# Performance work log

Measured on AMD Instinct MI355X. Metric: run time of the kernel, lower is better.

Reference implementation:

```python
import jax, jax.numpy as jnp
import numpy as np

EMBED, HEADS, FF, WIN = 512, 8, 2048, 64
SIGMA, PSTRENGTH, PERIOD, THRESH = 2.0, 1.0, 100.0, 0.0


def layer_norm(x, g, b, eps=1e-5):
    mu = jnp.mean(x, axis=-1, keepdims=True)
    var = jnp.var(x, axis=-1, keepdims=True)
    return (x - mu) * jax.lax.rsqrt(var + eps) * g + b


def setup_inputs() -> dict:
    key = jax.random.key(0)
    ks = jax.random.split(key, 16)
    s = 1.0 / np.sqrt(EMBED)
    sf = 1.0 / np.sqrt(FF)
    inp = {
        "src": jax.random.normal(ks[0], (8, 2048, EMBED), dtype=jnp.float32),
        "Wq": jax.random.normal(ks[1], (EMBED, EMBED), dtype=jnp.float32) * s,
        "bq": jnp.zeros((EMBED,), jnp.float32),
        "Wk": jax.random.normal(ks[2], (EMBED, EMBED), dtype=jnp.float32) * s,
        "bk": jnp.zeros((EMBED,), jnp.float32),
        "Wv": jax.random.normal(ks[3], (EMBED, EMBED), dtype=jnp.float32) * s,
        "bv": jnp.zeros((EMBED,), jnp.float32),
        "Wo": jax.random.normal(ks[4], (EMBED, EMBED), dtype=jnp.float32) * s,
        "bo": jnp.zeros((EMBED,), jnp.float32),
        "Wg": jax.random.normal(ks[5], (EMBED, 1), dtype=jnp.float32) * s,
        "bg": jnp.zeros((1,), jnp.float32),
        "W1": jax.random.normal(ks[6], (EMBED, FF), dtype=jnp.float32) * s,
        "b1": jnp.zeros((FF,), jnp.float32),
        "W2": jax.random.normal(ks[7], (FF, EMBED), dtype=jnp.float32) * sf,
        "b2": jnp.zeros((EMBED,), jnp.float32),
        "ln1_g": jnp.ones((EMBED,), jnp.float32),
        "ln1_b": jnp.zeros((EMBED,), jnp.float32),
        "ln2_g": jnp.ones((EMBED,), jnp.float32),
        "ln2_b": jnp.zeros((EMBED,), jnp.float32),
    }
    return inp


def gated_sparse_attn(x, Wq, bq, Wk, bk, Wv, bv, Wo, bo, Wg, bg):
    B, S, D = x.shape
    H, dh = HEADS, D // HEADS
    q = (x @ Wq + bq).reshape(B, S, H, dh).transpose(0, 2, 1, 3)  # [B,H,S,dh]
    k = (x @ Wk + bk).reshape(B, S, H, dh).transpose(0, 2, 1, 3)
    v = (x @ Wv + bv).reshape(B, S, H, dh).transpose(0, 2, 1, 3)
    scores = jnp.einsum('bhqd,bhkd->bhqk', q, k) / jnp.sqrt(jnp.float32(dh))
    idx = jnp.arange(S, dtype=jnp.float32)
    dist = idx[:, None] - idx[None, :]  # [S,S]
    gauss_bias = jnp.exp(-(dist * dist) / (2.0 * SIGMA * SIGMA))
    per_bias = PSTRENGTH * jnp.cos(2.0 * jnp.pi * dist / PERIOD)
    scores = scores + gauss_bias + per_bias  # positional biases baked into scores
    local = jnp.abs(dist) <= WIN  # local-window sparsity mask
    scores = jnp.where(local, scores, jnp.float32(-1e9))
    attn = jax.nn.softmax(scores, axis=-1)
    out = jnp.einsum('bhqk,bhkd->bhqd', attn, v)
    out = out.transpose(0, 2, 1, 3).reshape(B, S, D) @ Wo + bo
    gate = jax.nn.sigmoid(x @ Wg + bg)  # [B,S,1] learned gating
    gate = jnp.where(gate > THRESH, gate, jnp.float32(0.0))
    return gate * out


def reference(src, Wq, bq, Wk, bk, Wv, bv, Wo, bo, Wg, bg, W1, b1, W2, b2, ln1_g, ln1_b, ln2_g, ln2_b):
    # dropout is identity in eval mode
    attn_out = gated_sparse_attn(src, Wq, bq, Wk, bk, Wv, bv, Wo, bo, Wg, bg)
    x = layer_norm(src + attn_out, ln1_g, ln1_b)
    ff = jax.nn.relu(x @ W1 + b1) @ W2 + b2
    return layer_norm(x + ff, ln2_g, ln2_b)
```

## Files before the change

kernel.cpp:

```cpp
#include <hip/hip_runtime.h>
#include <hip/hip_bf16.h>
#include <math.h>

#define S_LEN   2048
#define D_MOD   512
#define N_HEADS 8
#define D_HEAD  64
#define FF_DIM  2048
#define M_ROWS  16384
#define BHSD    8388608

typedef __attribute__((ext_vector_type(8))) __bf16 bf16x8;
typedef __attribute__((ext_vector_type(4))) float  f32x4;
typedef unsigned short u16;

__device__ __forceinline__ u16 f2bf(float f) {
  unsigned u = __float_as_uint(f);
  u += 0x7fffu + ((u >> 16) & 1u);
  return (u16)(u >> 16);
}
__device__ __forceinline__ float bf2f(u16 h) { return __uint_as_float(((unsigned)h) << 16); }

__device__ __forceinline__ f32x4 mfma16(bf16x8 a, bf16x8 b, f32x4 c) {
  return __builtin_amdgcn_mfma_f32_16x16x32_bf16(a, b, c, 0, 0, 0);
}

__device__ __forceinline__ void async16(void* lds, const void* g) {
  __builtin_amdgcn_global_load_lds(
      (const __attribute__((address_space(1))) unsigned int*)g,
      (__attribute__((address_space(3))) unsigned int*)lds, 16, 0, 0);
}

#define BAR()    asm volatile("s_barrier" ::: "memory")
#define WAITV(n) asm volatile("s_waitcnt vmcnt(" #n ")" ::: "memory")
#define WAITL()  asm volatile("s_waitcnt lgkmcnt(0)" ::: "memory")

__device__ __forceinline__ int swz384(int row, int bir) {
  return row * 384 + ((bir & ~127) | ((bir ^ ((row & 7) << 4)) & 127));
}

__global__ __launch_bounds__(256) void cvt_gate(const float* __restrict__ src,
                                                const float* __restrict__ Wg,
                                                const float* __restrict__ bg,
                                                u16* __restrict__ xb,
                                                float* __restrict__ gate) {
  const int wid = threadIdx.x >> 6, lane = threadIdx.x & 63;
  const size_t row = (size_t)blockIdx.x * 4 + wid;
  const float4* s = reinterpret_cast<const float4*>(src + row * D_MOD);
  const float4* w = reinterpret_cast<const float4*>(Wg);
  float4 a0 = s[lane * 2], a1 = s[lane * 2 + 1];
  float4 w0 = w[lane * 2], w1 = w[lane * 2 + 1];
  float acc = a0.x * w0.x + a0.y * w0.y + a0.z * w0.z + a0.w * w0.w +
              a1.x * w1.x + a1.y * w1.y + a1.z * w1.z + a1.w * w1.w;
#pragma unroll
  for (int m = 1; m < 64; m <<= 1) acc += __shfl_xor(acc, m);
  ushort4 h0, h1;
  h0.x = f2bf(a0.x); h0.y = f2bf(a0.y); h0.z = f2bf(a0.z); h0.w = f2bf(a0.w);
  h1.x = f2bf(a1.x); h1.y = f2bf(a1.y); h1.z = f2bf(a1.z); h1.w = f2bf(a1.w);
  ushort4* ob = reinterpret_cast<ushort4*>(xb + row * D_MOD);
  ob[lane * 2] = h0; ob[lane * 2 + 1] = h1;
  if (lane == 0) {
    float g = 1.f / (1.f + __expf(-(acc + bg[0])));
    gate[row] = g > 0.f ? g : 0.f;
  }
}

__global__ void transpose_cvt(const float* __restrict__ in, u16* __restrict__ out,
                              int K, int N) {
  __shared__ float t[32][33];
  const int n0 = blockIdx.x * 32, k0 = blockIdx.y * 32;
  const int tx = threadIdx.x, ty = threadIdx.y;
#pragma unroll
  for (int i = 0; i < 4; ++i)
    t[ty + 8 * i][tx] = in[(size_t)(k0 + ty + 8 * i) * N + n0 + tx];
  __syncthreads();
#pragma unroll
  for (int i = 0; i < 4; ++i)
    out[(size_t)(n0 + ty + 8 * i) * K + k0 + tx] = f2bf(t[tx][ty + 8 * i]);
}

__global__ __launch_bounds__(256) void ln1red_k(const u16* __restrict__ xb,
                                                const float* __restrict__ gate,
                                                const u16* __restrict__ p0,
                                                const u16* __restrict__ p1,
                                                const float* __restrict__ bo,
                                                const float* __restrict__ gam,
                                                const float* __restrict__ bet,
                                                u16* __restrict__ outb) {
  const int wid = threadIdx.x >> 6, lane = threadIdx.x & 63;
  const size_t row = (size_t)blockIdx.x * 4 + wid;
  const size_t base = row * D_MOD;
  const float g = gate[row];
  const ushort4* sp = reinterpret_cast<const ushort4*>(xb + base);
  const ushort4* a  = reinterpret_cast<const ushort4*>(p0 + base);
  const ushort4* c  = reinterpret_cast<const ushort4*>(p1 + base);
  const float4*  bb = reinterpret_cast<const float4*>(bo);
  ushort4 s0 = sp[lane * 2], s1 = sp[lane * 2 + 1];
  ushort4 a0 = a[lane * 2], a1 = a[lane * 2 + 1];
  ushort4 c0 = c[lane * 2], c1 = c[lane * 2 + 1];
  float4 d0 = bb[lane * 2], d1 = bb[lane * 2 + 1];
  float4 v0, v1;
  v0.x = bf2f(s0.x) + g * (bf2f(a0.x) + bf2f(c0.x) + d0.x);
  v0.y = bf2f(s0.y) + g * (bf2f(a0.y) + bf2f(c0.y) + d0.y);
  v0.z = bf2f(s0.z) + g * (bf2f(a0.z) + bf2f(c0.z) + d0.z);
  v0.w = bf2f(s0.w) + g * (bf2f(a0.w) + bf2f(c0.w) + d0.w);
  v1.x = bf2f(s1.x) + g * (bf2f(a1.x) + bf2f(c1.x) + d1.x);
  v1.y = bf2f(s1.y) + g * (bf2f(a1.y) + bf2f(c1.y) + d1.y);
  v1.z = bf2f(s1.z) + g * (bf2f(a1.z) + bf2f(c1.z) + d1.z);
  v1.w = bf2f(s1.w) + g * (bf2f(a1.w) + bf2f(c1.w) + d1.w);
  float s  = v0.x + v0.y + v0.z + v0.w + v1.x + v1.y + v1.z + v1.w;
  float s2 = v0.x * v0.x + v0.y * v0.y + v0.z * v0.z + v0.w * v0.w +
             v1.x * v1.x + v1.y * v1.y + v1.z * v1.z + v1.w * v1.w;
#pragma unroll
  for (int m = 1; m < 64; m <<= 1) { s += __shfl_xor(s, m); s2 += __shfl_xor(s2, m); }
  const float mu = s * (1.0f / 512.0f);
  const float var = s2 * (1.0f / 512.0f) - mu * mu;
  const float rs = 1.0f / sqrtf(var + 1e-5f);
  const float4* gp = reinterpret_cast<const float4*>(gam);
  const float4* bp = reinterpret_cast<const float4*>(bet);
  float4 g0 = gp[lane * 2], g1 = gp[lane * 2 + 1];
  float4 e0 = bp[lane * 2], e1 = bp[lane * 2 + 1];
  ushort4 h0, h1;
  h0.x = f2bf((v0.x - mu) * rs * g0.x + e0.x);  h0.y = f2bf((v0.y - mu) * rs * g0.y + e0.y);
  h0.z = f2bf((v0.z - mu) * rs * g0.z + e0.z);  h0.w = f2bf((v0.w - mu) * rs * g0.w + e0.w);
  h1.x = f2bf((v1.x - mu) * rs * g1.x + e1.x);  h1.y = f2bf((v1.y - mu) * rs * g1.y + e1.y);
  h1.z = f2bf((v1.z - mu) * rs * g1.z + e1.z);  h1.w = f2bf((v1.w - mu) * rs * g1.w + e1.w);
  ushort4* ob = reinterpret_cast<ushort4*>(outb + base);
  ob[lane * 2] = h0; ob[lane * 2 + 1] = h1;
}

__global__ __launch_bounds__(256) void ln2red_k(const u16* __restrict__ xb,
                                                const u16* __restrict__ p0,
                                                const u16* __restrict__ p1,
                                                const float* __restrict__ b2,
                                                const float* __restrict__ gam,
                                                const float* __restrict__ bet,
                                                float* __restrict__ out) {
  const int wid = threadIdx.x >> 6, lane = threadIdx.x & 63;
  const size_t row = (size_t)blockIdx.x * 4 + wid;
  const size_t base = row * D_MOD;
  const ushort4* xp = reinterpret_cast<const ushort4*>(xb + base);
  const ushort4* q0 = reinterpret_cast<const ushort4*>(p0 + base);
  const ushort4* q1 = reinterpret_cast<const ushort4*>(p1 + base);
  const float4* bb = reinterpret_cast<const float4*>(b2);
  ushort4 h0 = xp[lane * 2], h1 = xp[lane * 2 + 1];
  ushort4 a0 = q0[lane * 2], a1 = q0[lane * 2 + 1];
  ushort4 c0 = q1[lane * 2], c1 = q1[lane * 2 + 1];
  float4 d0 = bb[lane * 2], d1 = bb[lane * 2 + 1];
  float4 v0, v1;
  v0.x = bf2f(h0.x) + bf2f(a0.x) + bf2f(c0.x) + d0.x;
  v0.y = bf2f(h0.y) + bf2f(a0.y) + bf2f(c0.y) + d0.y;
  v0.z = bf2f(h0.z) + bf2f(a0.z) + bf2f(c0.z) + d0.z;
  v0.w = bf2f(h0.w) + bf2f(a0.w) + bf2f(c0.w) + d0.w;
  v1.x = bf2f(h1.x) + bf2f(a1.x) + bf2f(c1.x) + d1.x;
  v1.y = bf2f(h1.y) + bf2f(a1.y) + bf2f(c1.y) + d1.y;
  v1.z = bf2f(h1.z) + bf2f(a1.z) + bf2f(c1.z) + d1.z;
  v1.w = bf2f(h1.w) + bf2f(a1.w) + bf2f(c1.w) + d1.w;
  float s  = v0.x + v0.y + v0.z + v0.w + v1.x + v1.y + v1.z + v1.w;
  float s2 = v0.x * v0.x + v0.y * v0.y + v0.z * v0.z + v0.w * v0.w +
             v1.x * v1.x + v1.y * v1.y + v1.z * v1.z + v1.w * v1.w;
#pragma unroll
  for (int m = 1; m < 64; m <<= 1) { s += __shfl_xor(s, m); s2 += __shfl_xor(s2, m); }
  const float mu = s * (1.0f / 512.0f);
  const float var = s2 * (1.0f / 512.0f) - mu * mu;
  const float rs = 1.0f / sqrtf(var + 1e-5f);
  const float4* gp = reinterpret_cast<const float4*>(gam);
  const float4* bp = reinterpret_cast<const float4*>(bet);
  float4 g0 = gp[lane * 2], g1 = gp[lane * 2 + 1];
  float4 e0 = bp[lane * 2], e1 = bp[lane * 2 + 1];
  float4 o0, o1;
  o0.x = (v0.x - mu) * rs * g0.x + e0.x;  o0.y = (v0.y - mu) * rs * g0.y + e0.y;
  o0.z = (v0.z - mu) * rs * g0.z + e0.z;  o0.w = (v0.w - mu) * rs * g0.w + e0.w;
  o1.x = (v1.x - mu) * rs * g1.x + e1.x;  o1.y = (v1.y - mu) * rs * g1.y + e1.y;
  o1.z = (v1.z - mu) * rs * g1.z + e1.z;  o1.w = (v1.w - mu) * rs * g1.w + e1.w;
  float4* q = reinterpret_cast<float4*>(out + base);
  q[lane * 2] = o0; q[lane * 2 + 1] = o1;
}

struct EpiArgs {
  const float* b0; const float* b1; const float* b2;
  float* outf; u16* outb; u16* outb2;
};

template<int EPI, int LD, int NT, int KSLICE, int GX, int GY>
__device__ __forceinline__ void gemm256_body(const u16* __restrict__ A,
                                             const u16* __restrict__ Bt, EpiArgs e) {
  extern __shared__ char smem[];
  char* Asb = smem;
  char* Bsb = smem + 65536;
  const int tid = threadIdx.x;
  const int wid = tid >> 6, lane = tid & 63;
  const int sub = lane >> 4, lc = lane & 15;
  const int wr = wid >> 2, wcn = wid & 3;

  const int nwg = (int)(gridDim.x * gridDim.y * gridDim.z);
  const int orig = ((int)blockIdx.z * (int)gridDim.y + (int)blockIdx.y) * (int)gridDim.x + (int)blockIdx.x;
  const int cpx = nwg >> 3;
  const int wg = (orig & 7) * cpx + (orig >> 3);
  const int bx = wg % GX;
  const int by = (wg / GX) % GY;
  const int bz = wg / (GX * GY);
  const int m0 = by * 256, n0 = bx * 256;
  const int kb = KSLICE * bz;

  const u16* Ab = A + (size_t)m0 * LD;
  const u16* Bb = Bt + (size_t)n0 * LD;

  f32x4 acc[8][4];
#pragma unroll
  for (int i = 0; i < 8; ++i)
#pragma unroll
    for (int j = 0; j < 4; ++j) acc[i][j] = (f32x4){0.f, 0.f, 0.f, 0.f};

  const int lr0 = tid >> 3;
  const int sl  = tid & 7;

#define STAGE(BASE, SRC, BUF, KT)                                              \
  {                                                                            \
    const int kk_ = kb + (KT) * 64;                                            \
    _Pragma("unroll")                                                          \
    for (int r_ = 0; r_ < 4; ++r_) {                                           \
      const int lr_ = r_ * 64 + lr0;                                           \
      async16((BASE) + (BUF) * 32768 + r_ * 8192 + wid * 1024,                 \
              (SRC) + (size_t)lr_ * LD + kk_ + ((sl ^ (lr_ & 7)) << 3));       \
    }                                                                          \
  }
#define LDFRAG(BASE, ROW, KS) \
  (*reinterpret_cast<const bf16x8*>((BASE) + (ROW) * 128 + ((((KS) * 64) + sub * 16) ^ (((ROW) & 7) << 4))))

  STAGE(Bsb, Bb, 0, 0);
  STAGE(Asb, Ab, 0, 0);
  STAGE(Bsb, Bb, 1, 1);
  STAGE(Asb, Ab, 1, 1);
  WAITV(8);
  BAR();

  for (int t = 0; t < NT; ++t) {
    const int buf = t & 1;
    char* Abl = Asb + buf * 32768;
    char* Bbl = Bsb + buf * 32768;
    bf16x8 af[4][2], bfr[2][2][2];
#pragma unroll
    for (int f = 0; f < 4; ++f) {
      const int row = wr * 128 + f * 16 + lc;
#pragma unroll
      for (int ks = 0; ks < 2; ++ks) af[f][ks] = LDFRAG(Abl, row, ks);
    }
#pragma unroll
    for (int f = 0; f < 2; ++f) {
      const int row = wcn * 64 + f * 16 + lc;
#pragma unroll
      for (int ks = 0; ks < 2; ++ks) bfr[0][f][ks] = LDFRAG(Bbl, row, ks);
    }
    __builtin_amdgcn_s_setprio(1);
#pragma unroll
    for (int f = 0; f < 4; ++f)
#pragma unroll
      for (int c = 0; c < 2; ++c)
#pragma unroll
        for (int ks = 0; ks < 2; ++ks)
          acc[f][c] = mfma16(af[f][ks], bfr[0][c][ks], acc[f][c]);
    __builtin_amdgcn_s_setprio(0);
    BAR();
#pragma unroll
    for (int f = 0; f < 2; ++f) {
      const int row = wcn * 64 + 32 + f * 16 + lc;
#pragma unroll
      for (int ks = 0; ks < 2; ++ks) bfr[1][f][ks] = LDFRAG(Bbl, row, ks);
    }
    __builtin_amdgcn_s_setprio(1);
#pragma unroll
    for (int f = 0; f < 4; ++f)
#pragma unroll
      for (int c = 0; c < 2; ++c)
#pragma unroll
        for (int ks = 0; ks < 2; ++ks)
          acc[f][2 + c] = mfma16(af[f][ks], bfr[1][c][ks], acc[f][2 + c]);
    __builtin_amdgcn_s_setprio(0);
    WAITL();
    BAR();
    if (t + 2 < NT) STAGE(Bsb, Bb, buf, t + 2);
#pragma unroll
    for (int f = 0; f < 4; ++f) {
      const int row = wr * 128 + 64 + f * 16 + lc;
#pragma unroll
      for (int ks = 0; ks < 2; ++ks) af[f][ks] = LDFRAG(Abl, row, ks);
    }
    __builtin_amdgcn_s_setprio(1);
#pragma unroll
    for (int f = 0; f < 4; ++f)
#pragma unroll
      for (int c = 0; c < 2; ++c)
#pragma unroll
        for (int ks = 0; ks < 2; ++ks)
          acc[4 + f][2 + c] = mfma16(af[f][ks], bfr[1][c][ks], acc[4 + f][2 + c]);
    __builtin_amdgcn_s_setprio(0);
    WAITL();
    BAR();
    if (t + 2 < NT) STAGE(Asb, Ab, buf, t + 2);
    __builtin_amdgcn_s_setprio(1);
#pragma unroll
    for (int f = 0; f < 4; ++f)
#pragma unroll
      for (int c = 0; c < 2; ++c)
#pragma unroll
        for (int ks = 0; ks < 2; ++ks)
          acc[4 + f][c] = mfma16(af[f][ks], bfr[0][c][ks], acc[4 + f][c]);
    __builtin_amdgcn_s_setprio(0);
    if (t + 1 < NT) {
      if (t + 2 < NT) { WAITV(8); } else { WAITV(0); }
      BAR();
    }
  }
#undef STAGE
#undef LDFRAG

  if constexpr (EPI == 2 || EPI == 4) {
#pragma unroll
    for (int fr = 0; fr < 8; ++fr) {
      const int row0 = m0 + wr * 128 + fr * 16 + sub * 4;
#pragma unroll
      for (int fc = 0; fc < 4; ++fc) {
        const int col = n0 + wcn * 64 + fc * 16 + lc;
        f32x4 v = acc[fr][fc];
#pragma unroll
        for (int i = 0; i < 4; ++i) {
          const int row = row0 + i;
          const float val = v[i];
          if constexpr (EPI == 2) {
            float o = val + e.b0[col];
            e.outb[(size_t)row * FF_DIM + col] = f2bf(o > 0.f ? o : 0.f);
          } else {
            u16* dst = (bz == 0) ? e.outb : e.outb2;
            dst[(size_t)row * D_MOD + col] = f2bf(val);
          }
        }
      }
    }
  } else {
    const int which = n0 >> 9;
    const int bbi = m0 >> 11, ss0 = m0 & 2047;
    if (which == 2) {
      __syncthreads();
      u16* Cs = reinterpret_cast<u16*>(smem);
      const int nnb = n0 & 511;
#pragma unroll
      for (int fr = 0; fr < 8; ++fr) {
        const int lrow = wr * 128 + fr * 16 + sub * 4;
#pragma unroll
        for (int fc = 0; fc < 4; ++fc) {
          const int lcol = wcn * 64 + fc * 16 + lc;
          const float bias = e.b2[nnb + lcol];
          f32x4 v = acc[fr][fc];
#pragma unroll
          for (int i = 0; i < 4; ++i) {
            const int row = lrow + i;
            const int sbyte = (row * 2) ^ ((lcol & 7) << 4);
            *reinterpret_cast<u16*>((char*)Cs + lcol * 512 + sbyte) = f2bf(v[i] + bias);
          }
        }
      }
      __syncthreads();
#pragma unroll
      for (int p = 0; p < 16; ++p) {
        const int off = p * 8192 + tid * 16;
        const int nn = off >> 9, cb = off & 511;
        const int cbs = cb ^ ((nn & 7) << 4);
        uint4 v = *reinterpret_cast<const uint4*>((const char*)Cs + nn * 512 + cbs);
        const int nng = nnb + nn;
        const int hh = nng >> 6, dd = nng & 63;
        *reinterpret_cast<uint4*>(
            (char*)(e.outb2 + (((size_t)bbi * N_HEADS + hh) * D_HEAD + dd) * S_LEN + ss0) + cb) = v;
      }
    } else {
#pragma unroll
      for (int fr = 0; fr < 8; ++fr) {
        const int row0 = m0 + wr * 128 + fr * 16 + sub * 4;
        const int ss = row0 & 2047;
#pragma unroll
        for (int fc = 0; fc < 4; ++fc) {
          const int col = n0 + wcn * 64 + fc * 16 + lc;
          const int nn = col & 511;
          const int hh = nn >> 6, dd = nn & 63;
          const float* bp = (which == 0) ? e.b0 : e.b1;
          const float bias = bp[nn];
          f32x4 v = acc[fr][fc];
#pragma unroll
          for (int i = 0; i < 4; ++i)
            e.outb[(size_t)which * BHSD +
                   (((size_t)bbi * N_HEADS + hh) * S_LEN + ss + i) * D_HEAD + dd]
                = f2bf(v[i] + bias);
        }
      }
    }
  }
}

__global__ __launch_bounds__(512, 2) void k_qkv(const u16* __restrict__ A, const u16* __restrict__ B, EpiArgs e) {
  gemm256_body<0, 512, 8, 0, 6, 64>(A, B, e);
}
__global__ __launch_bounds__(512, 2) void k_ff1(const u16* __restrict__ A, const u16* __restrict__ B, EpiArgs e) {
  gemm256_body<2, 512, 8, 0, 8, 64>(A, B, e);
}
__global__ __launch_bounds__(512, 2) void k_ff2(const u16* __restrict__ A, const u16* __restrict__ B, EpiArgs e) {
  gemm256_body<4, 2048, 16, 1024, 2, 64>(A, B, e);
}
__global__ __launch_bounds__(512, 2) void k_proj(const u16* __restrict__ A, const u16* __restrict__ B, EpiArgs e) {
  gemm256_body<4, 512, 4, 256, 2, 64>(A, B, e);
}

__global__ __launch_bounds__(256)
void attn_k(const u16* __restrict__ Q, const u16* __restrict__ Kt,
            const u16* __restrict__ VTg, u16* __restrict__ Oflat) {
  __shared__ __align__(16) u16 VT[64 * 192];
  __shared__ __align__(16) u16 P [64 * 192];
  __shared__ float tab[256];
  const int tid = threadIdx.x;
  const int wid = tid >> 6, lane = tid & 63;
  const int sub = lane >> 4, lc = lane & 15;
  const int qb = blockIdx.x, bh = blockIdx.y;
  const int bb = bh >> 3, hh = bh & 7;
  const int q0 = qb * 64, kstart = q0 - 64;
  const u16* Qb = Q  + (size_t)bh * S_LEN * D_HEAD;
  const u16* Kb = Kt + (size_t)bh * S_LEN * D_HEAD;
  const u16* Vtb = VTg + (size_t)bh * D_HEAD * S_LEN;

#pragma unroll
  for (int it = 0; it < 6; ++it) {
    const int c = (wid * 6 + it) * 64 + lane;
    const int row = c / 24;
    const int bir = (c % 24) * 16;
    const int swz = (bir & ~127) | ((bir ^ ((row & 7) << 4)) & 127);
    int sb = kstart + (swz >> 1);
    sb = sb < 0 ? 0 : (sb > S_LEN - 8 ? S_LEN - 8 : sb);
    async16((char*)VT + (wid * 6 + it) * 1024, Vtb + (size_t)row * S_LEN + sb);
  }

  if (tid < 255) {
    const int di = tid - 127;
    const float fd = (float)di;
    tab[tid] = (di >= -64 && di <= 64)
        ? __expf(-fd * fd * 0.125f) + __cosf(0.06283185307179586f * fd)
        : -1e9f;
  }

  bf16x8 qf[2];
#pragma unroll
  for (int ks = 0; ks < 2; ++ks)
    qf[ks] = *reinterpret_cast<const bf16x8*>(Qb + (size_t)(q0 + wid * 16 + lc) * D_HEAD + ks * 32 + sub * 8);

  f32x4 sc[12];
#pragma unroll
  for (int t = 0; t < 12; ++t) sc[t] = (f32x4){0.f, 0.f, 0.f, 0.f};
#pragma unroll
  for (int ks = 0; ks < 2; ++ks)
#pragma unroll
    for (int t = 0; t < 12; ++t) {
      int kg = kstart + t * 16 + lc;
      int kc = kg < 0 ? 0 : (kg > S_LEN - 1 ? S_LEN - 1 : kg);
      bf16x8 kf = *reinterpret_cast<const bf16x8*>(Kb + (size_t)kc * D_HEAD + ks * 32 + sub * 8);
      sc[t] = mfma16(qf[ks], kf, sc[t]);
    }
  __syncthreads();

  float rmax[4] = {-3e38f, -3e38f, -3e38f, -3e38f};
#pragma unroll
  for (int t = 0; t < 12; ++t) {
    const int kk = t * 16 + lc;
    const int kg = kstart + kk;
    const bool valid = (kg >= 0) && (kg < S_LEN);
#pragma unroll
    for (int r = 0; r < 4; ++r) {
      const int qrow = wid * 16 + sub * 4 + r;
      const float bias = valid ? tab[qrow - kk + 191] : -1e9f;
      const float sv = sc[t][r] * 0.125f + bias;
      sc[t][r] = sv;
      rmax[r] = fmaxf(rmax[r], sv);
    }
  }
#pragma unroll
  for (int m = 1; m < 16; m <<= 1)
#pragma unroll
    for (int r = 0; r < 4; ++r) rmax[r] = fmaxf(rmax[r], __shfl_xor(rmax[r], m));
  float rsum[4] = {0.f, 0.f, 0.f, 0.f};
#pragma unroll
  for (int t = 0; t < 12; ++t)
#pragma unroll
    for (int r = 0; r < 4; ++r) {
      const float p = __expf(sc[t][r] - rmax[r]);
      sc[t][r] = p; rsum[r] += p;
    }
#pragma unroll
  for (int m = 1; m < 16; m <<= 1)
#pragma unroll
    for (int r = 0; r < 4; ++r) rsum[r] += __shfl_xor(rsum[r], m);
  float rinv[4];
#pragma unroll
  for (int r = 0; r < 4; ++r) rinv[r] = 1.0f / rsum[r];
#pragma unroll
  for (int t = 0; t < 12; ++t)
#pragma unroll
    for (int r = 0; r < 4; ++r) {
      const int qrow = wid * 16 + sub * 4 + r;
      *reinterpret_cast<u16*>(reinterpret_cast<char*>(P) + swz384(qrow, (t * 16 + lc) * 2))
          = f2bf(sc[t][r] * rinv[r]);
    }
  __syncthreads();

  f32x4 oacc[4];
#pragma unroll
  for (int t = 0; t < 4; ++t) oacc[t] = (f32x4){0.f, 0.f, 0.f, 0.f};
  const int arow = wid * 16 + lc;
#pragma unroll
  for (int ks = 0; ks < 6; ++ks) {
    const int bir = ks * 64 + sub * 16;
    bf16x8 pa = *reinterpret_cast<const bf16x8*>(reinterpret_cast<char*>(P) + swz384(arow, bir));
#pragma unroll
    for (int t = 0; t < 4; ++t) {
      bf16x8 vb = *reinterpret_cast<const bf16x8*>(reinterpret_cast<char*>(VT) + swz384(t * 16 + lc, bir));
      oacc[t] = mfma16(pa, vb, oacc[t]);
    }
  }

  const size_t obase = ((size_t)bb * S_LEN + q0) * D_MOD + hh * D_HEAD;
#pragma unroll
  for (int t = 0; t < 4; ++t)
#pragma unroll
    for (int r = 0; r < 4; ++r) {
      const int qrow = wid * 16 + sub * 4 + r;
      Oflat[obase + (size_t)qrow * D_MOD + t * 16 + lc] = f2bf(oacc[t][r]);
    }
}

extern "C" void kernel_launch(void* const* d_in, const int* in_sizes, int n_in,
                              void* d_out, int out_size, void* d_ws, size_t ws_size,
                              hipStream_t stream) {
  (void)in_sizes; (void)n_in; (void)out_size; (void)ws_size;
  const float* src  = (const float*)d_in[0];
  const float* Wq   = (const float*)d_in[1];
  const float* bq   = (const float*)d_in[2];
  const float* Wk   = (const float*)d_in[3];
  const float* bk   = (const float*)d_in[4];
  const float* Wv   = (const float*)d_in[5];
  const float* bv   = (const float*)d_in[6];
  const float* Wo   = (const float*)d_in[7];
  const float* bo   = (const float*)d_in[8];
  const float* Wg   = (const float*)d_in[9];
  const float* bg   = (const float*)d_in[10];
  const float* W1   = (const float*)d_in[11];
  const float* b1   = (const float*)d_in[12];
  const float* W2   = (const float*)d_in[13];
  const float* b2   = (const float*)d_in[14];
  const float* ln1g = (const float*)d_in[15];
  const float* ln1b = (const float*)d_in[16];
  const float* ln2g = (const float*)d_in[17];
  const float* ln2b = (const float*)d_in[18];
  float* out = (float*)d_out;

  char* ws = (char*)d_ws;
  u16*   WqkvT  = (u16*)  (ws + 0);
  u16*   WoT    = (u16*)  (ws + 1572864);
  u16*   W1T    = (u16*)  (ws + 2097152);
  u16*   W2T    = (u16*)  (ws + 4194304);
  float* gatef  = (float*)(ws + 6291456);
  u16*   Xbf    = (u16*)  (ws + 6356992);
  u16*   QKVbf  = (u16*)  (ws + 23134208);
  u16*   attnfl = (u16*)  (ws + 73465856);
  u16*   pr0    = (u16*)  (ws + 90243072);
  u16*   pr1    = (u16*)  (ws + 107020288);
  u16*   xbf2   = (u16*)  (ws + 123797504);
  u16*   VTg    = (u16*)  (ws + 140574720);
  u16*   hbuf   = Xbf;
  u16*   pf0    = pr0;
  u16*   pf1    = pr1;

  (void)hipFuncSetAttribute((const void*)k_qkv,  hipFuncAttributeMaxDynamicSharedMemorySize, 131072);
  (void)hipFuncSetAttribute((const void*)k_ff1,  hipFuncAttributeMaxDynamicSharedMemorySize, 131072);
  (void)hipFuncSetAttribute((const void*)k_ff2,  hipFuncAttributeMaxDynamicSharedMemorySize, 131072);
  (void)hipFuncSetAttribute((const void*)k_proj, hipFuncAttributeMaxDynamicSharedMemorySize, 131072);

  dim3 tb(32, 8);
  cvt_gate<<<4096, 256, 0, stream>>>(src, Wg, bg, Xbf, gatef);
  transpose_cvt<<<dim3(16, 16), tb, 0, stream>>>(Wq, WqkvT,             512, 512);
  transpose_cvt<<<dim3(16, 16), tb, 0, stream>>>(Wk, WqkvT + 512 * 512, 512, 512);
  transpose_cvt<<<dim3(16, 16), tb, 0, stream>>>(Wv, WqkvT + 2 * 512 * 512, 512, 512);
  transpose_cvt<<<dim3(16, 16), tb, 0, stream>>>(Wo, WoT, 512, 512);
  transpose_cvt<<<dim3(64, 16), tb, 0, stream>>>(W1, W1T, 512, 2048);
  transpose_cvt<<<dim3(16, 64), tb, 0, stream>>>(W2, W2T, 2048, 512);

  EpiArgs e1{bq, bk, bv, nullptr, QKVbf, VTg};
  k_qkv<<<dim3(6, 64, 1), 512, 131072, stream>>>(Xbf, WqkvT, e1);

  attn_k<<<dim3(32, 64), 256, 0, stream>>>(QKVbf, QKVbf + BHSD, VTg, attnfl);

  EpiArgs e2{nullptr, nullptr, nullptr, nullptr, pr0, pr1};
  k_proj<<<dim3(2, 64, 2), 512, 131072, stream>>>(attnfl, WoT, e2);

  ln1red_k<<<4096, 256, 0, stream>>>(Xbf, gatef, pr0, pr1, bo, ln1g, ln1b, xbf2);

  EpiArgs e3{b1, nullptr, nullptr, nullptr, hbuf, nullptr};
  k_ff1<<<dim3(8, 64, 1), 512, 131072, stream>>>(xbf2, W1T, e3);

  EpiArgs e4{nullptr, nullptr, nullptr, nullptr, pf0, pf1};
  k_ff2<<<dim3(2, 64, 2), 512, 131072, stream>>>(hbuf, W2T, e4);

  ln2red_k<<<4096, 256, 0, stream>>>(xbf2, pf0, pf1, b2, ln2g, ln2b, out);
}
```

Baseline: 215.5 us.

## Add single-buffered GEMM variant with 64KB LDS for higher occupancy in proj/FF

Adds a DBUF template flag to the 256x256 GEMM body. The new single-buffered path stages one K-tile, waits, computes, then loads the next tile. k_proj, k_ff1 and k_ff2 now use it with 64KB dynamic LDS and launch_bounds(512,4), trading intra-block load/compute overlap for more resident workgroups per CU. The risk is exposed global-load latency and register pressure under the tighter occupancy bound, since 128 accumulator floats per thread may spill.

```diff
diff --git a/kernel.cpp b/kernel.cpp
--- a/kernel.cpp
+++ b/kernel.cpp
@@ -182,12 +182,12 @@
   float* outf; u16* outb; u16* outb2;
 };
 
-template<int EPI, int LD, int NT, int KSLICE, int GX, int GY>
+template<int EPI, int LD, int NT, int KSLICE, int GX, int GY, int DBUF>
 __device__ __forceinline__ void gemm256_body(const u16* __restrict__ A,
                                              const u16* __restrict__ Bt, EpiArgs e) {
   extern __shared__ char smem[];
   char* Asb = smem;
-  char* Bsb = smem + 65536;
+  char* Bsb = smem + (DBUF ? 65536 : 32768);
   const int tid = threadIdx.x;
   const int wid = tid >> 6, lane = tid & 63;
   const int sub = lane >> 4, lc = lane & 15;
@@ -228,88 +228,137 @@
 #define LDFRAG(BASE, ROW, KS) \
   (*reinterpret_cast<const bf16x8*>((BASE) + (ROW) * 128 + ((((KS) * 64) + sub * 16) ^ (((ROW) & 7) << 4))))
 
-  STAGE(Bsb, Bb, 0, 0);
-  STAGE(Asb, Ab, 0, 0);
-  STAGE(Bsb, Bb, 1, 1);
-  STAGE(Asb, Ab, 1, 1);
-  WAITV(8);
-  BAR();
-
-  for (int t = 0; t < NT; ++t) {
-    const int buf = t & 1;
-    char* Abl = Asb + buf * 32768;
-    char* Bbl = Bsb + buf * 32768;
-    bf16x8 af[4][2], bfr[2][2][2];
-#pragma unroll
-    for (int f = 0; f < 4; ++f) {
-      const int row = wr * 128 + f * 16 + lc;
-#pragma unroll
-      for (int ks = 0; ks < 2; ++ks) af[f][ks] = LDFRAG(Abl, row, ks);
-    }
-#pragma unroll
-    for (int f = 0; f < 2; ++f) {
-      const int row = wcn * 64 + f * 16 + lc;
-#pragma unroll
-      for (int ks = 0; ks < 2; ++ks) bfr[0][f][ks] = LDFRAG(Bbl, row, ks);
-    }
-    __builtin_amdgcn_s_setprio(1);
-#pragma unroll
-    for (int f = 0; f < 4; ++f)
-#pragma unroll
-      for (int c = 0; c < 2; ++c)
-#pragma unroll
-        for (int ks = 0; ks < 2; ++ks)
-          acc[f][c] = mfma16(af[f][ks], bfr[0][c][ks], acc[f][c]);
-    __builtin_amdgcn_s_setprio(0);
+  if constexpr (DBUF) {
+    STAGE(Bsb, Bb, 0, 0);
+    STAGE(Asb, Ab, 0, 0);
+    STAGE(Bsb, Bb, 1, 1);
+    STAGE(Asb, Ab, 1, 1);
+    WAITV(8);
     BAR();
-#pragma unroll
-    for (int f = 0; f < 2; ++f) {
-      const int row = wcn * 64 + 32 + f * 16 + lc;
-#pragma unroll
-      for (int ks = 0; ks < 2; ++ks) bfr[1][f][ks] = LDFRAG(Bbl, row, ks);
-    }
-    __builtin_amdgcn_s_setprio(1);
-#pragma unroll
-    for (int f = 0; f < 4; ++f)
-#pragma unroll
-      for (int c = 0; c < 2; ++c)
-#pragma unroll
-        for (int ks = 0; ks < 2; ++ks)
-          acc[f][2 + c] = mfma16(af[f][ks], bfr[1][c][ks], acc[f][2 + c]);
-    __builtin_amdgcn_s_setprio(0);
-    WAITL();
-    BAR();
-    if (t + 2 < NT) STAGE(Bsb, Bb, buf, t + 2);
-#pragma unroll
-    for (int f = 0; f < 4; ++f) {
-      const int row = wr * 128 + 64 + f * 16 + lc;
-#pragma unroll
-      for (int ks = 0; ks < 2; ++ks) af[f][ks] = LDFRAG(Abl, row, ks);
-    }
-    __builtin_amdgcn_s_setprio(1);
-#pragma unroll
-    for (int f = 0; f < 4; ++f)
-#pragma unroll
-      for (int c = 0; c < 2; ++c)
-#pragma unroll
-        for (int ks = 0; ks < 2; ++ks)
-          acc[4 + f][2 + c] = mfma16(af[f][ks], bfr[1][c][ks], acc[4 + f][2 + c]);
-    __builtin_amdgcn_s_setprio(0);
-    WAITL();
-    BAR();
-    if (t + 2 < NT) STAGE(Asb, Ab, buf, t + 2);
-    __builtin_amdgcn_s_setprio(1);
-#pragma unroll
-    for (int f = 0; f < 4; ++f)
-#pragma unroll
-      for (int c = 0; c < 2; ++c)
-#pragma unroll
-        for (int ks = 0; ks < 2; ++ks)
-          acc[4 + f][c] = mfma16(af[f][ks], bfr[0][c][ks], acc[4 + f][c]);
-    __builtin_amdgcn_s_setprio(0);
-    if (t + 1 < NT) {
-      if (t + 2 < NT) { WAITV(8); } else { WAITV(0); }
+
+    for (int t = 0; t < NT; ++t) {
+      const int buf = t & 1;
+      char* Abl = Asb + buf * 32768;
+      char* Bbl = Bsb + buf * 32768;
+      bf16x8 af[4][2], bfr[2][2][2];
+#pragma unroll
+      for (int f = 0; f < 4; ++f) {
+        const int row = wr * 128 + f * 16 + lc;
+#pragma unroll
+        for (int ks = 0; ks < 2; ++ks) af[f][ks] = LDFRAG(Abl, row, ks);
+      }
+#pragma unroll
+      for (int f = 0; f < 2; ++f) {
+        const int row = wcn * 64 + f * 16 + lc;
+#pragma unroll
+        for (int ks = 0; ks < 2; ++ks) bfr[0][f][ks] = LDFRAG(Bbl, row, ks);
+      }
+      __builtin_amdgcn_s_setprio(1);
+#pragma unroll
+      for (int f = 0; f < 4; ++f)
+#pragma unroll
+        for (int c = 0; c < 2; ++c)
+#pragma unroll
+          for (int ks = 0; ks < 2; ++ks)
+            acc[f][c] = mfma16(af[f][ks], bfr[0][c][ks], acc[f][c]);
+      __builtin_amdgcn_s_setprio(0);
       BAR();
+#pragma unroll
+      for (int f = 0; f < 2; ++f) {
+        const int row = wcn * 64 + 32 + f * 16 + lc;
+#pragma unroll
+        for (int ks = 0; ks < 2; ++ks) bfr[1][f][ks] = LDFRAG(Bbl, row, ks);
+      }
+      __builtin_amdgcn_s_setprio(1);
+#pragma unroll
+      for (int f = 0; f < 4; ++f)
+#pragma unroll
+        for (int c = 0; c < 2; ++c)
+#pragma unroll
+          for (int ks = 0; ks < 2; ++ks)
+            acc[f][2 + c] = mfma16(af[f][ks], bfr[1][c][ks], acc[f][2 + c]);
+      __builtin_amdgcn_s_setprio(0);
+      WAITL();
+      BAR();
+      if (t + 2 < NT) STAGE(Bsb, Bb, buf, t + 2);
+#pragma unroll
+      for (int f = 0; f < 4; ++f) {
+        const int row = wr * 128 + 64 + f * 16 + lc;
+#pragma unroll
+        for (int ks = 0; ks < 2; ++ks) af[f][ks] = LDFRAG(Abl, row, ks);
+      }
+      __builtin_amdgcn_s_setprio(1);
+#pragma unroll
+      for (int f = 0; f < 4; ++f)
+#pragma unroll
+        for (int c = 0; c < 2; ++c)
+#pragma unroll
+          for (int ks = 0; ks < 2; ++ks)
+            acc[4 + f][2 + c] = mfma16(af[f][ks], bfr[1][c][ks], acc[4 + f][2 + c]);
+      __builtin_amdgcn_s_setprio(0);
+      WAITL();
+      BAR();
+      if (t + 2 < NT) STAGE(Asb, Ab, buf, t + 2);
+      __builtin_amdgcn_s_setprio(1);
+#pragma unroll
+      for (int f = 0; f < 4; ++f)
+#pragma unroll
+        for (int c = 0; c < 2; ++c)
+#pragma unroll
+          for (int ks = 0; ks < 2; ++ks)
+            acc[4 + f][c] = mfma16(af[f][ks], bfr[0][c][ks], acc[4 + f][c]);
+      __builtin_amdgcn_s_setprio(0);
+      if (t + 1 < NT) {
+        if (t + 2 < NT) { WAITV(8); } else { WAITV(0); }
+        BAR();
+      }
+    }
+  } else {
+    STAGE(Bsb, Bb, 0, 0);
+    STAGE(Asb, Ab, 0, 0);
+    for (int t = 0; t < NT; ++t) {
+      WAITV(0);
+      BAR();
+      bf16x8 af[4][2], bfr[2][2][2];
+#pragma unroll
+      for (int f = 0; f < 2; ++f)
+#pragma unroll
+        for (int ks = 0; ks < 2; ++ks) {
+          bfr[0][f][ks] = LDFRAG(Bsb, wcn * 64 + f * 16 + lc, ks);
+          bfr[1][f][ks] = LDFRAG(Bsb, wcn * 64 + 32 + f * 16 + lc, ks);
+        }
+#pragma unroll
+      for (int f = 0; f < 4; ++f)
+#pragma unroll
+        for (int ks = 0; ks < 2; ++ks) af[f][ks] = LDFRAG(Asb, wr * 128 + f * 16 + lc, ks);
+      __builtin_amdgcn_s_setprio(1);
+#pragma unroll
+      for (int f = 0; f < 4; ++f)
+#pragma unroll
+        for (int j = 0; j < 4; ++j)
+#pragma unroll
+          for (int ks = 0; ks < 2; ++ks)
+            acc[f][j] = mfma16(af[f][ks], bfr[j >> 1][j & 1][ks], acc[f][j]);
+      __builtin_amdgcn_s_setprio(0);
+#pragma unroll
+      for (int f = 0; f < 4; ++f)
+#pragma unroll
+        for (int ks = 0; ks < 2; ++ks) af[f][ks] = LDFRAG(Asb, wr * 128 + 64 + f * 16 + lc, ks);
+      __builtin_amdgcn_s_setprio(1);
+#pragma unroll
+      for (int f = 0; f < 4; ++f)
+#pragma unroll
+        for (int j = 0; j < 4; ++j)
+#pragma unroll
+          for (int ks = 0; ks < 2; ++ks)
+            acc[4 + f][j] = mfma16(af[f][ks], bfr[j >> 1][j & 1][ks], acc[4 + f][j]);
+      __builtin_amdgcn_s_setprio(0);
+      WAITL();
+      BAR();
+      if (t + 1 < NT) {
+        STAGE(Bsb, Bb, 0, t + 1);
+        STAGE(Asb, Ab, 0, t + 1);
+      }
     }
   }
 #undef STAGE
@@ -397,16 +446,16 @@
 }
 
 __global__ __launch_bounds__(512, 2) void k_qkv(const u16* __restrict__ A, const u16* __restrict__ B, EpiArgs e) {
-  gemm256_body<0, 512, 8, 0, 6, 64>(A, B, e);
-}
-__global__ __launch_bounds__(512, 2) void k_ff1(const u16* __restrict__ A, const u16* __restrict__ B, EpiArgs e) {
-  gemm256_body<2, 512, 8, 0, 8, 64>(A, B, e);
-}
-__global__ __launch_bounds__(512, 2) void k_ff2(const u16* __restrict__ A, const u16* __restrict__ B, EpiArgs e) {
-  gemm256_body<4, 2048, 16, 1024, 2, 64>(A, B, e);
-}
-__global__ __launch_bounds__(512, 2) void k_proj(const u16* __restrict__ A, const u16* __restrict__ B, EpiArgs e) {
-  gemm256_body<4, 512, 4, 256, 2, 64>(A, B, e);
+  gemm256_body<0, 512, 8, 0, 6, 64, 1>(A, B, e);
+}
+__global__ __launch_bounds__(512, 4) void k_ff1(const u16* __restrict__ A, const u16* __restrict__ B, EpiArgs e) {
+  gemm256_body<2, 512, 8, 0, 8, 64, 0>(A, B, e);
+}
+__global__ __launch_bounds__(512, 4) void k_ff2(const u16* __restrict__ A, const u16* __restrict__ B, EpiArgs e) {
+  gemm256_body<4, 2048, 16, 1024, 2, 64, 0>(A, B, e);
+}
+__global__ __launch_bounds__(512, 4) void k_proj(const u16* __restrict__ A, const u16* __restrict__ B, EpiArgs e) {
+  gemm256_body<4, 512, 4, 256, 2, 64, 0>(A, B, e);
 }
 
 __global__ __launch_bounds__(256)
@@ -575,9 +624,9 @@
   u16*   pf1    = pr1;
 
   (void)hipFuncSetAttribute((const void*)k_qkv,  hipFuncAttributeMaxDynamicSharedMemorySize, 131072);
-  (void)hipFuncSetAttribute((const void*)k_ff1,  hipFuncAttributeMaxDynamicSharedMemorySize, 131072);
-  (void)hipFuncSetAttribute((const void*)k_ff2,  hipFuncAttributeMaxDynamicSharedMemorySize, 131072);
-  (void)hipFuncSetAttribute((const void*)k_proj, hipFuncAttributeMaxDynamicSharedMemorySize, 131072);
+  (void)hipFuncSetAttribute((const void*)k_ff1,  hipFuncAttributeMaxDynamicSharedMemorySize, 65536);
+  (void)hipFuncSetAttribute((const void*)k_ff2,  hipFuncAttributeMaxDynamicSharedMemorySize, 65536);
+  (void)hipFuncSetAttribute((const void*)k_proj, hipFuncAttributeMaxDynamicSharedMemorySize, 65536);
 
   dim3 tb(32, 8);
   cvt_gate<<<4096, 256, 0, stream>>>(src, Wg, bg, Xbf, gatef);
@@ -594,15 +643,15 @@
   attn_k<<<dim3(32, 64), 256, 0, stream>>>(QKVbf, QKVbf + BHSD, VTg, attnfl);
 
   EpiArgs e2{nullptr, nullptr, nullptr, nullptr, pr0, pr1};
-  k_proj<<<dim3(2, 64, 2), 512, 131072, stream>>>(attnfl, WoT, e2);
+  k_proj<<<dim3(2, 64, 2), 512, 65536, stream>>>(attnfl, WoT, e2);
 
   ln1red_k<<<4096, 256, 0, stream>>>(Xbf, gatef, pr0, pr1, bo, ln1g, ln1b, xbf2);
 
   EpiArgs e3{b1, nullptr, nullptr, nullptr, hbuf, nullptr};
-  k_ff1<<<dim3(8, 64, 1), 512, 131072, stream>>>(xbf2, W1T, e3);
+  k_ff1<<<dim3(8, 64, 1), 512, 65536, stream>>>(xbf2, W1T, e3);
 
   EpiArgs e4{nullptr, nullptr, nullptr, nullptr, pf0, pf1};
-  k_ff2<<<dim3(2, 64, 2), 512, 131072, stream>>>(hbuf, W2T, e4);
+  k_ff2<<<dim3(2, 64, 2), 512, 65536, stream>>>(hbuf, W2T, e4);
 
   ln2red_k<<<4096, 256, 0, stream>>>(xbf2, pf0, pf1, b2, ln2g, ln2b, out);
 }
```

New measurement: 693.9 us. +222.1%, slower.
